# Performance work log

Measured on AMD Instinct MI355X. Metric: run time of the kernel, lower is better.

## Reference

```python
import jax, jax.numpy as jnp
import numpy as np

B, N, DIM = 2, 2048, 2048
H, KVH, HD = 16, 4, 128
N_REP = H // KVH
SCALE = np.float32(HD ** -0.5)


def setup_inputs() -> dict:
    key = jax.random.key(0)
    ks = jax.random.split(key, 5)
    x = jax.random.normal(ks[0], (B, N, DIM), dtype=jnp.float32)
    mask = jnp.tril(jnp.ones((N, N), dtype=jnp.int32))[None, None]  # [1,1,N,N] causal
    Wq = jax.random.normal(ks[1], (DIM, H * HD), dtype=jnp.float32) * (DIM ** -0.5)
    Wk = jax.random.normal(ks[2], (DIM, KVH * HD), dtype=jnp.float32) * (DIM ** -0.5)
    Wv = jax.random.normal(ks[3], (DIM, KVH * HD), dtype=jnp.float32) * (DIM ** -0.5)
    Wo = jax.random.normal(ks[4], (H * HD, DIM), dtype=jnp.float32) * ((H * HD) ** -0.5)
    return {"x": x, "mask": mask, "Wq": Wq, "Wk": Wk, "Wv": Wv, "Wo": Wo}


def reference(x, mask, Wq, Wk, Wv, Wo):
    Bx, Nx, _ = x.shape
    # projections -> [B, heads, N, head_dim]
    q = (x @ Wq).reshape(Bx, Nx, H, HD).transpose(0, 2, 1, 3)
    k = (x @ Wk).reshape(Bx, Nx, KVH, HD).transpose(0, 2, 1, 3)
    v = (x @ Wv).reshape(Bx, Nx, KVH, HD).transpose(0, 2, 1, 3)
    # repeat_interleave KV heads to match query heads (GQA)
    k = jnp.repeat(k, N_REP, axis=1)
    v = jnp.repeat(v, N_REP, axis=1)
    attn = jnp.einsum('bhqd,bhkd->bhqk', q, k) * SCALE
    attn = jnp.where(mask == 0, jnp.float32(-jnp.inf), attn)
    attn = jax.nn.softmax(attn, axis=-1)
    out = jnp.einsum('bhqk,bhkd->bhqd', attn, v)
    out = out.transpose(0, 2, 1, 3).reshape(Bx, Nx, H * HD)
    return out @ Wo
```

## Files before the change

kernel.cpp:

```cpp
#include <hip/hip_runtime.h>
#include <hip/hip_bf16.h>
#include <math.h>

typedef __bf16 bf16;
typedef bf16 bf16x8 __attribute__((ext_vector_type(8)));
typedef bf16 bf16x4v __attribute__((ext_vector_type(4)));
typedef float f32x4 __attribute__((ext_vector_type(4)));

#define GLD16(g, l) __builtin_amdgcn_global_load_lds(                          \
    (__attribute__((address_space(1))) void*)(g),                              \
    (__attribute__((address_space(3))) void*)(l), 16, 0, 0)

#define MFMA16(a, b, c) __builtin_amdgcn_mfma_f32_16x16x32_bf16((a), (b), (c), 0, 0, 0)

#if __has_builtin(__builtin_amdgcn_exp2f)
#define EXP2F(x) __builtin_amdgcn_exp2f(x)
#else
#define EXP2F(x) exp2f(x)
#endif

__device__ __forceinline__ f32x4 shfl_xor4(f32x4 a, int m) {
  f32x4 r;
  #pragma unroll
  for (int i = 0; i < 4; i++) r[i] = __shfl_xor(a[i], m);
  return r;
}

__global__ void cast_f32_bf16(const float* __restrict__ in, bf16* __restrict__ out, int n4) {
  int i = blockIdx.x * blockDim.x + threadIdx.x;
  if (i < n4) {
    float4 v = ((const float4*)in)[i];
    bf16x4v o;
    o.x = (bf16)v.x; o.y = (bf16)v.y; o.z = (bf16)v.z; o.w = (bf16)v.w;
    ((bf16x4v*)out)[i] = o;
  }
}

__global__ void transpose_cast(const float* __restrict__ in, bf16* __restrict__ out,
                               int colsIn, int outStride, int outRowOff, float scale) {
  __shared__ float t[32][33];
  int c0 = blockIdx.x * 32, r0 = blockIdx.y * 32;
  int tx = threadIdx.x, ty = threadIdx.y;
  #pragma unroll
  for (int i = 0; i < 32; i += 8)
    t[ty + i][tx] = in[(size_t)(r0 + ty + i) * colsIn + (c0 + tx)];
  __syncthreads();
  #pragma unroll
  for (int i = 0; i < 32; i += 8)
    out[(size_t)(outRowOff + c0 + ty + i) * outStride + (r0 + tx)] = (bf16)(t[tx][ty + i] * scale);
}

__global__ void transpose_v(const bf16* __restrict__ QKV, bf16* __restrict__ Vg) {
  __shared__ bf16 t[32][34];
  int n0 = blockIdx.x * 32, d0 = blockIdx.y * 32;
  int bk = blockIdx.z;
  int b = bk >> 2, kvh = bk & 3;
  const bf16* src = QKV + (size_t)b * 2048 * 3072 + 2560 + kvh * 128;
  bf16* dst = Vg + (size_t)bk * 128 * 2048;
  int tx = threadIdx.x, ty = threadIdx.y;
  #pragma unroll
  for (int i = 0; i < 32; i += 8)
    t[ty + i][tx] = src[(size_t)(n0 + ty + i) * 3072 + (d0 + tx)];
  __syncthreads();
  #pragma unroll
  for (int i = 0; i < 32; i += 8)
    dst[(size_t)(d0 + ty + i) * 2048 + (n0 + tx)] = t[tx][ty + i];
}

template <typename OutT>
__global__ __launch_bounds__(256, 2) void gemm_bt(const bf16* __restrict__ A,
                                                  const bf16* __restrict__ Bt,
                                                  OutT* __restrict__ C,
                                                  int M, int N, int K) {
  __shared__ __attribute__((aligned(16))) bf16 As[128 * 32];
  __shared__ __attribute__((aligned(16))) bf16 Bs[128 * 32];
  const int tid = threadIdx.x;
  const int lane = tid & 63;
  const int wave = tid >> 6;
  const int wm = wave >> 1, wn = wave & 1;
  const int l15 = lane & 15, quad = lane >> 4;
  const int rowBase = blockIdx.y * 128;
  const int colBase = blockIdx.x * 128;

  f32x4 acc[4][4] = {};

  const int cb0 = wave * 64;
  const int c0 = cb0 + lane;
  const int c1 = c0 + 256;
  const bf16* a0 = A + (size_t)(rowBase + (c0 >> 2)) * K + (c0 & 3) * 8;
  const bf16* a1 = A + (size_t)(rowBase + (c1 >> 2)) * K + (c1 & 3) * 8;
  const bf16* b0 = Bt + (size_t)(colBase + (c0 >> 2)) * K + (c0 & 3) * 8;
  const bf16* b1 = Bt + (size_t)(colBase + (c1 >> 2)) * K + (c1 & 3) * 8;
  bf16* lA0 = &As[cb0 * 8];
  bf16* lA1 = &As[(cb0 + 256) * 8];
  bf16* lB0 = &Bs[cb0 * 8];
  bf16* lB1 = &Bs[(cb0 + 256) * 8];

  for (int k0 = 0; k0 < K; k0 += 32) {
    GLD16(a0 + k0, lA0);
    GLD16(a1 + k0, lA1);
    GLD16(b0 + k0, lB0);
    GLD16(b1 + k0, lB1);
    __syncthreads();
    bf16x8 af[4], bfr[4];
    #pragma unroll
    for (int i = 0; i < 4; i++)
      af[i] = *(const bf16x8*)&As[(wm * 64 + i * 16 + l15) * 32 + quad * 8];
    #pragma unroll
    for (int i = 0; i < 4; i++)
      bfr[i] = *(const bf16x8*)&Bs[(wn * 64 + i * 16 + l15) * 32 + quad * 8];
    #pragma unroll
    for (int i = 0; i < 4; i++)
      #pragma unroll
      for (int j = 0; j < 4; j++)
        acc[i][j] = MFMA16(af[i], bfr[j], acc[i][j]);
    __syncthreads();
  }

  #pragma unroll
  for (int i = 0; i < 4; i++) {
    int row = rowBase + wm * 64 + i * 16 + quad * 4;
    #pragma unroll
    for (int j = 0; j < 4; j++) {
      int col = colBase + wn * 64 + j * 16 + l15;
      #pragma unroll
      for (int r = 0; r < 4; r++)
        C[(size_t)(row + r) * N + col] = (OutT)acc[i][j][r];
    }
  }
}

#define MASKV (-1e30f)

__device__ const unsigned char BMAP[22] = {
  28, 58, 24, 50, 20, 46, 36, 32,
  62, 59, 54, 51, 47, 42, 55, 63,
  0, 4, 8, 12, 16, 43
};

#define SLOT_F32 16640

__global__ __launch_bounds__(256, 2) void gqa_attn(const bf16* __restrict__ QKV,
                                                   const bf16* __restrict__ Vg,
                                                   bf16* __restrict__ Obf,
                                                   float* __restrict__ Part) {
  __shared__ __attribute__((aligned(16))) bf16 Kl[64 * 128];
  __shared__ __attribute__((aligned(16))) bf16 Vt[128 * 64];
  __shared__ __attribute__((aligned(16))) bf16 Pl[4][32 * 68];

  const int tid = threadIdx.x;
  const int lane = tid & 63;
  const int wave = tid >> 6;
  const int l15 = lane & 15, quad = lane >> 4;

  const int e = BMAP[blockIdx.x >> 5];
  const int bh = blockIdx.x & 31;
  const int qt = e >> 2;
  const int split = (e >> 1) & 1;
  const int half = e & 1;
  const int b = bh >> 4, h = bh & 15, kvh = h >> 2;
  const int q0 = qt * 128;
  const int nkt = 2 * qt + 2;
  const int kt_lo = (split && half) ? (nkt >> 1) : 0;
  const int kt_hi = (split && !half) ? (nkt >> 1) : nkt;

  const size_t rs = 3072;
  const bf16* Qb  = QKV + (size_t)b * 2048 * rs + h * 128;
  const bf16* Kb  = QKV + (size_t)b * 2048 * rs + 2048 + kvh * 128;
  const bf16* Vgb = Vg + (size_t)(b * 4 + kvh) * 128 * 2048;

  bf16x8 qf[2][4];
  #pragma unroll
  for (int mt = 0; mt < 2; mt++) {
    int row = q0 + wave * 32 + mt * 16 + l15;
    #pragma unroll
    for (int ks = 0; ks < 4; ks++)
      qf[mt][ks] = *(const bf16x8*)&Qb[(size_t)row * rs + ks * 32 + quad * 8];
  }

  const bf16* kp[4]; const bf16* vp[4];
  bf16* kl[4]; bf16* vl[4];
  #pragma unroll
  for (int t = 0; t < 4; t++) {
    int keyl = wave * 16 + t * 4 + (lane >> 4);
    int ck = (lane & 15) ^ (4 * (t & 1) + (lane >> 4));
    kp[t] = Kb + (size_t)(kt_lo * 64 + keyl) * rs + ck * 8;
    kl[t] = &Kl[(wave * 16 + t * 4) * 128];
    int dl = wave * 32 + t * 8 + (lane >> 3);
    int cv = (lane & 7) ^ (lane >> 3);
    vp[t] = Vgb + (size_t)dl * 2048 + kt_lo * 64 + cv * 8;
    vl[t] = &Vt[(wave * 32 + t * 8) * 64];
  }

  f32x4 oacc[2][8] = {};
  f32x4 mrow[2], lrow[2];
  #pragma unroll
  for (int mt = 0; mt < 2; mt++)
    #pragma unroll
    for (int r = 0; r < 4; r++) { mrow[mt][r] = MASKV; lrow[mt][r] = 0.f; }

  const int myrow_hi = q0 + wave * 32 + 31;
  for (int kt = kt_lo; kt < kt_hi; kt++) {
    const int k0 = kt * 64;
    __syncthreads();
    #pragma unroll
    for (int t = 0; t < 4; t++) { GLD16(kp[t], kl[t]); kp[t] += 64 * rs; }
    #pragma unroll
    for (int t = 0; t < 4; t++) { GLD16(vp[t], vl[t]); vp[t] += 64; }
    __syncthreads();

    if (k0 > myrow_hi) continue;

    f32x4 s[2][4] = {};
    #pragma unroll
    for (int ks = 0; ks < 4; ks++) {
      #pragma unroll
      for (int nt = 0; nt < 4; nt++) {
        bf16x8 kf = *(const bf16x8*)&Kl[(nt * 16 + l15) * 128 +
                                        (((ks * 4 + quad) ^ (l15 & 7)) * 8)];
        s[0][nt] = MFMA16(qf[0][ks], kf, s[0][nt]);
        s[1][nt] = MFMA16(qf[1][ks], kf, s[1][nt]);
      }
    }
    if (kt >= nkt - 2) {
      #pragma unroll
      for (int mt = 0; mt < 2; mt++) {
        int rowb = q0 + wave * 32 + mt * 16 + quad * 4;
        #pragma unroll
        for (int nt = 0; nt < 4; nt++) {
          int col = k0 + nt * 16 + l15;
          #pragma unroll
          for (int r = 0; r < 4; r++)
            if (col > rowb + r) s[mt][nt][r] = MASKV;
        }
      }
    }
    #pragma unroll
    for (int mt = 0; mt < 2; mt++) {
      f32x4 mx = s[mt][0];
      #pragma unroll
      for (int nt = 1; nt < 4; nt++)
        #pragma unroll
        for (int r = 0; r < 4; r++) mx[r] = fmaxf(mx[r], s[mt][nt][r]);
      #pragma unroll
      for (int d = 1; d < 16; d <<= 1) {
        f32x4 o = shfl_xor4(mx, d);
        #pragma unroll
        for (int r = 0; r < 4; r++) mx[r] = fmaxf(mx[r], o[r]);
      }
      f32x4 mnew, alpha;
      #pragma unroll
      for (int r = 0; r < 4; r++) {
        mnew[r] = fmaxf(mrow[mt][r], mx[r]);
        alpha[r] = EXP2F(mrow[mt][r] - mnew[r]);
      }
      f32x4 rsum = {0.f, 0.f, 0.f, 0.f};
      #pragma unroll
      for (int nt = 0; nt < 4; nt++)
        #pragma unroll
        for (int r = 0; r < 4; r++) {
          float p = EXP2F(s[mt][nt][r] - mnew[r]);
          s[mt][nt][r] = p;
          rsum[r] += p;
        }
      #pragma unroll
      for (int d = 1; d < 16; d <<= 1) rsum += shfl_xor4(rsum, d);
      #pragma unroll
      for (int r = 0; r < 4; r++) {
        lrow[mt][r] = lrow[mt][r] * alpha[r] + rsum[r];
        mrow[mt][r] = mnew[r];
      }
      #pragma unroll
      for (int no = 0; no < 8; no++)
        #pragma unroll
        for (int r = 0; r < 4; r++) oacc[mt][no][r] *= alpha[r];
      #pragma unroll
      for (int nt = 0; nt < 4; nt++)
        #pragma unroll
        for (int r = 0; r < 4; r++)
          Pl[wave][(mt * 16 + quad * 4 + r) * 68 + nt * 16 + l15] = (bf16)s[mt][nt][r];
    }
    #pragma unroll
    for (int ks2 = 0; ks2 < 2; ks2++) {
      bf16x8 pf0 = *(const bf16x8*)&Pl[wave][l15 * 68 + ks2 * 32 + quad * 8];
      bf16x8 pf1 = *(const bf16x8*)&Pl[wave][(16 + l15) * 68 + ks2 * 32 + quad * 8];
      #pragma unroll
      for (int no = 0; no < 8; no++) {
        bf16x8 vf = *(const bf16x8*)&Vt[(no * 16 + l15) * 64 +
                                        (((ks2 * 4 + quad) ^ (l15 & 7)) * 8)];
        oacc[0][no] = MFMA16(pf0, vf, oacc[0][no]);
        oacc[1][no] = MFMA16(pf1, vf, oacc[1][no]);
      }
    }
  }

  if (!split) {
    #pragma unroll
    for (int mt = 0; mt < 2; mt++) {
      f32x4 linv;
      #pragma unroll
      for (int r = 0; r < 4; r++) linv[r] = 1.0f / lrow[mt][r];
      int row = q0 + wave * 32 + mt * 16 + quad * 4;
      #pragma unroll
      for (int no = 0; no < 8; no++) {
        int col = h * 128 + no * 16 + l15;
        #pragma unroll
        for (int r = 0; r < 4; r++)
          Obf[(size_t)(b * 2048 + row + r) * 2048 + col] = (bf16)(oacc[mt][no][r] * linv[r]);
      }
    }
  } else {
    const int fidx = bh * 6 + (qt - 10);
    float* slot = Part + (size_t)(fidx * 2 + half) * SLOT_F32;
    #pragma unroll
    for (int mt = 0; mt < 2; mt++) {
      int row = wave * 32 + mt * 16 + quad * 4;
      #pragma unroll
      for (int no = 0; no < 8; no++) {
        int col = no * 16 + l15;
        #pragma unroll
        for (int r = 0; r < 4; r++)
          slot[(row + r) * 128 + col] = oacc[mt][no][r];
      }
    }
    if (l15 == 0) {
      #pragma unroll
      for (int mt = 0; mt < 2; mt++)
        #pragma unroll
        for (int r = 0; r < 4; r++) {
          int row = wave * 32 + mt * 16 + quad * 4 + r;
          slot[16384 + row] = mrow[mt][r];
          slot[16512 + row] = lrow[mt][r];
        }
    }
  }
}

__global__ __launch_bounds__(256) void merge_split(const float* __restrict__ Part,
                                                   bf16* __restrict__ Obf) {
  const int fidx = blockIdx.x;
  const int bh = fidx / 6, qt = 10 + fidx % 6;
  const int b = bh >> 4, h = bh & 15;
  const int tid = threadIdx.x;
  const int cl = (tid & 31) * 4;
  const int r0 = tid >> 5;
  const float* s0 = Part + (size_t)(fidx * 2) * SLOT_F32;
  const float* s1 = s0 + SLOT_F32;
  #pragma unroll
  for (int i = 0; i < 16; i++) {
    int row = r0 + i * 8;
    float m0 = s0[16384 + row], l0 = s0[16512 + row];
    float m1 = s1[16384 + row], l1 = s1[16512 + row];
    float ms = fmaxf(m0, m1);
    float a0 = EXP2F(m0 - ms), a1 = EXP2F(m1 - ms);
    float linv = 1.0f / (l0 * a0 + l1 * a1);
    f32x4 v0 = *(const f32x4*)&s0[row * 128 + cl];
    f32x4 v1 = *(const f32x4*)&s1[row * 128 + cl];
    bf16x4v o;
    #pragma unroll
    for (int r = 0; r < 4; r++) o[r] = (bf16)((v0[r] * a0 + v1[r] * a1) * linv);
    *(bf16x4v*)&Obf[(size_t)(b * 2048 + qt * 128 + row) * 2048 + h * 128 + cl] = o;
  }
}

extern "C" void kernel_launch(void* const* d_in, const int* in_sizes, int n_in,
                              void* d_out, int out_size, void* d_ws, size_t ws_size,
                              hipStream_t stream) {
  const float* x  = (const float*)d_in[0];
  const float* Wq = (const float*)d_in[2];
  const float* Wk = (const float*)d_in[3];
  const float* Wv = (const float*)d_in[4];
  const float* Wo = (const float*)d_in[5];
  float* out = (float*)d_out;

  bf16* Xb    = (bf16*)d_ws;
  bf16* Wqkvt = Xb + 8388608;
  bf16* Wot   = Wqkvt + 6291456;
  bf16* QKV   = Wot + 4194304;
  bf16* Obf   = QKV + 12582912;
  bf16* Vg    = Obf + 8388608;

  float* Part = (float*)d_ws;

  const float qscale = (float)(0.08838834764831845 * 1.4426950408889634);

  cast_f32_bf16<<<8192, 256, 0, stream>>>(x, Xb, 2097152);
  dim3 tb(32, 8);
  transpose_cast<<<dim3(64, 64), tb, 0, stream>>>(Wq, Wqkvt, 2048, 2048, 0, qscale);
  transpose_cast<<<dim3(16, 64), tb, 0, stream>>>(Wk, Wqkvt, 512, 2048, 2048, 1.0f);
  transpose_cast<<<dim3(16, 64), tb, 0, stream>>>(Wv, Wqkvt, 512, 2048, 2560, 1.0f);
  transpose_cast<<<dim3(64, 64), tb, 0, stream>>>(Wo, Wot, 2048, 2048, 0, 1.0f);

  gemm_bt<bf16><<<dim3(24, 32), 256, 0, stream>>>(Xb, Wqkvt, QKV, 4096, 3072, 2048);
  transpose_v<<<dim3(64, 4, 8), tb, 0, stream>>>(QKV, Vg);
  gqa_attn<<<704, 256, 0, stream>>>(QKV, Vg, Obf, Part);
  merge_split<<<192, 256, 0, stream>>>(Part, Obf);
  gemm_bt<float><<<dim3(16, 32), 256, 0, stream>>>(Obf, Wot, out, 4096, 2048, 2048);
}
```

Measured before the change: 337.0 us.

## Use lazy softmax rescaling and compute row sums via MFMA with ones

Replaces the per-tile shuffle reduction of softmax row sums with an MFMA against a ones vector on the bf16 P fragments, so the denominator accumulates in the matrix unit. Rescaling of the output accumulators is also skipped unless some row's max grows by more than 8 in log2 units, checked wave-wide. This removes shuffles and the multiplies across 64 accumulators on most tiles, but sums the bf16-rounded probabilities and allows unrescaled exponents up to 2^8, which slightly changes numerics.

```diff
diff --git a/kernel.cpp b/kernel.cpp
--- a/kernel.cpp
+++ b/kernel.cpp
@@ -178,6 +178,10 @@
       qf[mt][ks] = *(const bf16x8*)&Qb[(size_t)row * rs + ks * 32 + quad * 8];
   }
 
+  bf16x8 ones8;
+  #pragma unroll
+  for (int i = 0; i < 8; i++) ones8[i] = (bf16)1.0f;
+
   const bf16* kp[4]; const bf16* vp[4];
   bf16* kl[4]; bf16* vl[4];
   #pragma unroll
@@ -193,11 +197,12 @@
   }
 
   f32x4 oacc[2][8] = {};
-  f32x4 mrow[2], lrow[2];
+  f32x4 lacc[2] = {};
+  f32x4 mrow[2];
   #pragma unroll
   for (int mt = 0; mt < 2; mt++)
     #pragma unroll
-    for (int r = 0; r < 4; r++) { mrow[mt][r] = MASKV; lrow[mt][r] = 0.f; }
+    for (int r = 0; r < 4; r++) mrow[mt][r] = MASKV;
 
   const int myrow_hi = q0 + wave * 32 + 31;
   for (int kt = kt_lo; kt < kt_hi; kt++) {
@@ -248,42 +253,37 @@
         #pragma unroll
         for (int r = 0; r < 4; r++) mx[r] = fmaxf(mx[r], o[r]);
       }
-      f32x4 mnew, alpha;
-      #pragma unroll
-      for (int r = 0; r < 4; r++) {
-        mnew[r] = fmaxf(mrow[mt][r], mx[r]);
-        alpha[r] = EXP2F(mrow[mt][r] - mnew[r]);
-      }
-      f32x4 rsum = {0.f, 0.f, 0.f, 0.f};
+      bool noresc = (mx[0] <= mrow[mt][0] + 8.f) && (mx[1] <= mrow[mt][1] + 8.f) &&
+                    (mx[2] <= mrow[mt][2] + 8.f) && (mx[3] <= mrow[mt][3] + 8.f);
+      if (!__all(noresc)) {
+        f32x4 alpha;
+        #pragma unroll
+        for (int r = 0; r < 4; r++) {
+          float mn = fmaxf(mrow[mt][r], mx[r]);
+          alpha[r] = EXP2F(mrow[mt][r] - mn);
+          mrow[mt][r] = mn;
+        }
+        #pragma unroll
+        for (int no = 0; no < 8; no++)
+          #pragma unroll
+          for (int r = 0; r < 4; r++) oacc[mt][no][r] *= alpha[r];
+        #pragma unroll
+        for (int r = 0; r < 4; r++) lacc[mt][r] *= alpha[r];
+      }
       #pragma unroll
       for (int nt = 0; nt < 4; nt++)
         #pragma unroll
         for (int r = 0; r < 4; r++) {
-          float p = EXP2F(s[mt][nt][r] - mnew[r]);
-          s[mt][nt][r] = p;
-          rsum[r] += p;
+          float p = EXP2F(s[mt][nt][r] - mrow[mt][r]);
+          Pl[wave][(mt * 16 + quad * 4 + r) * 68 + nt * 16 + l15] = (bf16)p;
         }
-      #pragma unroll
-      for (int d = 1; d < 16; d <<= 1) rsum += shfl_xor4(rsum, d);
-      #pragma unroll
-      for (int r = 0; r < 4; r++) {
-        lrow[mt][r] = lrow[mt][r] * alpha[r] + rsum[r];
-        mrow[mt][r] = mnew[r];
-      }
-      #pragma unroll
-      for (int no = 0; no < 8; no++)
-        #pragma unroll
-        for (int r = 0; r < 4; r++) oacc[mt][no][r] *= alpha[r];
-      #pragma unroll
-      for (int nt = 0; nt < 4; nt++)
-        #pragma unroll
-        for (int r = 0; r < 4; r++)
-          Pl[wave][(mt * 16 + quad * 4 + r) * 68 + nt * 16 + l15] = (bf16)s[mt][nt][r];
     }
     #pragma unroll
     for (int ks2 = 0; ks2 < 2; ks2++) {
       bf16x8 pf0 = *(const bf16x8*)&Pl[wave][l15 * 68 + ks2 * 32 + quad * 8];
       bf16x8 pf1 = *(const bf16x8*)&Pl[wave][(16 + l15) * 68 + ks2 * 32 + quad * 8];
+      lacc[0] = MFMA16(pf0, ones8, lacc[0]);
+      lacc[1] = MFMA16(pf1, ones8, lacc[1]);
       #pragma unroll
       for (int no = 0; no < 8; no++) {
         bf16x8 vf = *(const bf16x8*)&Vt[(no * 16 + l15) * 64 +
@@ -299,7 +299,7 @@
     for (int mt = 0; mt < 2; mt++) {
       f32x4 linv;
       #pragma unroll
-      for (int r = 0; r < 4; r++) linv[r] = 1.0f / lrow[mt][r];
+      for (int r = 0; r < 4; r++) linv[r] = 1.0f / lacc[mt][r];
       int row = q0 + wave * 32 + mt * 16 + quad * 4;
       #pragma unroll
       for (int no = 0; no < 8; no++) {
@@ -330,7 +330,7 @@
         for (int r = 0; r < 4; r++) {
           int row = wave * 32 + mt * 16 + quad * 4 + r;
           slot[16384 + row] = mrow[mt][r];
-          slot[16512 + row] = lrow[mt][r];
+          slot[16512 + row] = lacc[mt][r];
         }
     }
   }
```

Result: no change. 330.9 us (-1.8%).
